# Kernel tuning notes

Measured on AMD Instinct MI355X. Metric: run time of the kernel, lower is better.

## Reference

```python
import jax, jax.numpy as jnp
import numpy as np

# Dimensions
O, D, F_LSOA = 128, 128, 64      # origins, destinations, LSOA feature dim
T, FE, H = 128, 16, 64           # max seq len, edge_feature_dim, gru_hidden
NH, NO, PH = 128, 64, 128        # node_hidden, node_out, pair_hidden
P = O * D                        # number of O-D pairs


def _mlp3(x, W1, b1, W2, b2, W3, b3):
    # Linear->ReLU->Linear->ReLU->Linear (dropout is identity in eval mode)
    h = jax.nn.relu(x @ W1 + b1)
    h = jax.nn.relu(h @ W2 + b2)
    return h @ W3 + b3


def setup_inputs() -> dict:
    key = jax.random.key(0)
    ks = jax.random.split(key, 32)

    def rn(k, shape, s):
        return jax.random.normal(k, shape, dtype=jnp.float32) * s

    inp = {
        "O_feats": rn(ks[0], (O, F_LSOA), 1.0),
        "D_feats": rn(ks[1], (D, F_LSOA), 1.0),
        "seqs": rn(ks[2], (P, T, FE), 1.0),
        "lengths": jax.random.randint(ks[3], (P,), 1, T + 1, dtype=jnp.int32),
        # enc_O
        "WO1": rn(ks[4], (F_LSOA, NH), 0.05), "bO1": jnp.zeros((NH,), jnp.float32),
        "WO2": rn(ks[5], (NH, NH), 0.05),     "bO2": jnp.zeros((NH,), jnp.float32),
        "WO3": rn(ks[6], (NH, NO), 0.05),     "bO3": jnp.zeros((NO,), jnp.float32),
        # enc_D
        "WD1": rn(ks[7], (F_LSOA, NH), 0.05), "bD1": jnp.zeros((NH,), jnp.float32),
        "WD2": rn(ks[8], (NH, NH), 0.05),     "bD2": jnp.zeros((NH,), jnp.float32),
        "WD3": rn(ks[9], (NH, NO), 0.05),     "bD3": jnp.zeros((NO,), jnp.float32),
        # pair_head: 2*node_out -> pair_hidden -> 1
        "Wp1": rn(ks[10], (2 * NO, PH), 0.05), "bp1": jnp.zeros((PH,), jnp.float32),
        "Wp2": rn(ks[11], (PH, 1), 0.05),      "bp2": jnp.zeros((1,), jnp.float32),
        # GRU (gate order r, z, n as in PyTorch)
        "W_ih": rn(ks[12], (FE, 3 * H), 0.1),  "b_ih": jnp.zeros((3 * H,), jnp.float32),
        "W_hh": rn(ks[13], (H, 3 * H), 0.1),   "b_hh": jnp.zeros((3 * H,), jnp.float32),
        # seq_head
        "Ws": rn(ks[14], (H, 1), 0.1),         "bs": jnp.zeros((1,), jnp.float32),
    }
    return inp


def reference(O_feats, D_feats, seqs, lengths,
              WO1, bO1, WO2, bO2, WO3, bO3,
              WD1, bD1, WD2, bD2, WD3, bD3,
              Wp1, bp1, Wp2, bp2,
              W_ih, W_hh, b_ih, b_hh,
              Ws, bs):
    # Node encoders
    eo = _mlp3(O_feats, WO1, bO1, WO2, bO2, WO3, bO3)   # [O, NO]
    ed = _mlp3(D_feats, WD1, bD1, WD2, bD2, WD3, bD3)   # [D, NO]

    # Pairwise score: concat(eo, ed) -> MLP -> softplus
    pair_in = jnp.concatenate([
        jnp.broadcast_to(eo[:, None, :], (O, D, NO)),
        jnp.broadcast_to(ed[None, :, :], (O, D, NO)),
    ], axis=-1)                                          # [O, D, 2*NO]
    hp = jax.nn.relu(pair_in @ Wp1 + bp1)                # [O, D, PH]
    z_pair = (hp @ Wp2 + bp2)[..., 0]                    # [O, D]
    s_pair = jax.nn.softplus(z_pair)

    # Length-masked GRU over all O*D padded sequences (equiv. to pack_padded)
    xT = jnp.swapaxes(seqs, 0, 1)                        # [T, P, FE]
    h0 = jnp.zeros((P, H), jnp.float32)

    def step(h, inp):
        xt, t = inp
        gx = xt @ W_ih + b_ih                            # [P, 3H]
        gh = h @ W_hh + b_hh                             # [P, 3H]
        xr, xz, xn = jnp.split(gx, 3, axis=-1)
        hr, hz, hn = jnp.split(gh, 3, axis=-1)
        r = jax.nn.sigmoid(xr + hr)
        zg = jax.nn.sigmoid(xz + hz)
        n = jnp.tanh(xn + r * hn)
        h_new = (1.0 - zg) * n + zg * h
        h = jnp.where((t < lengths)[:, None], h_new, h)  # freeze past seq end
        return h, None

    h_last, _ = jax.lax.scan(step, h0, (xT, jnp.arange(T)))  # [P, H]

    p_seq = jax.nn.sigmoid(h_last @ Ws + bs)[:, 0].reshape(O, D)
    return jnp.sum(s_pair * p_seq)
```

## Files before the change

### kernel.cpp

```cpp
#include <hip/hip_runtime.h>
#include <hip/hip_bf16.h>

#define O_N 128
#define D_N 128
#define F_LS 64
#define T_MAX 128
#define FE_N 16
#define H_GRU 64
#define NH 128
#define NO 64
#define PH 128
#define NG 1024

typedef _Float16 f16;
typedef f16 f16x8 __attribute__((ext_vector_type(8)));
typedef float f32x4 __attribute__((ext_vector_type(4)));

__device__ __forceinline__ float fast_sigmoid(float x) {
    return __builtin_amdgcn_rcpf(1.f + __expf(-x));
}

__global__ __launch_bounds__(128) void k_enc(
    const float* __restrict__ O_feats, const float* __restrict__ D_feats,
    const float* __restrict__ WO1, const float* __restrict__ bO1,
    const float* __restrict__ WO2, const float* __restrict__ bO2,
    const float* __restrict__ WO3, const float* __restrict__ bO3,
    const float* __restrict__ WD1, const float* __restrict__ bD1,
    const float* __restrict__ WD2, const float* __restrict__ bD2,
    const float* __restrict__ WD3, const float* __restrict__ bD3,
    const float* __restrict__ Wp1,
    float* __restrict__ PA, float* __restrict__ PB, float* __restrict__ d_out)
{
    __shared__ float h1[NH];
    __shared__ float h2[NH];
    __shared__ float ev[NO];
    const int b = blockIdx.x;
    const int enc = b >> 7;
    const int row = b & 127;
    const int t = threadIdx.x;
    if (b == 0 && t == 0) d_out[0] = 0.f;

    const float* x  = (enc ? D_feats : O_feats) + row * F_LS;
    const float* W1 = enc ? WD1 : WO1;  const float* b1 = enc ? bD1 : bO1;
    const float* W2 = enc ? WD2 : WO2;  const float* b2 = enc ? bD2 : bO2;
    const float* W3 = enc ? WD3 : WO3;  const float* b3 = enc ? bD3 : bO3;

    float a = b1[t];
    #pragma unroll 8
    for (int k = 0; k < F_LS; ++k) a += x[k] * W1[k * NH + t];
    h1[t] = fmaxf(a, 0.f);
    __syncthreads();

    a = b2[t];
    #pragma unroll 8
    for (int k = 0; k < NH; ++k) a += h1[k] * W2[k * NH + t];
    h2[t] = fmaxf(a, 0.f);
    __syncthreads();

    if (t < NO) {
        a = b3[t];
        #pragma unroll 8
        for (int k = 0; k < NH; ++k) a += h2[k] * W3[k * NO + t];
        ev[t] = a;
    }
    __syncthreads();

    const float* Wp = Wp1 + (enc ? NO * PH : 0);
    a = 0.f;
    #pragma unroll 8
    for (int k = 0; k < NO; ++k) a += ev[k] * Wp[k * PH + t];
    (enc ? PB : PA)[row * PH + t] = a;
}

__global__ __launch_bounds__(128) void k_pair(
    const float* __restrict__ PA, const float* __restrict__ PB,
    const float* __restrict__ bp1, const float* __restrict__ Wp2,
    const float* __restrict__ bp2, float* __restrict__ s_pair)
{
    const int i = blockIdx.x;
    const int j = threadIdx.x;
    __shared__ float pa[PH];
    __shared__ float b1s[PH];
    __shared__ float w2s[PH];
    pa[j]  = PA[i * PH + j];
    b1s[j] = bp1[j];
    w2s[j] = Wp2[j];
    __syncthreads();
    const float* pb = PB + j * PH;
    float acc = 0.f;
    #pragma unroll 8
    for (int c = 0; c < PH; ++c)
        acc += w2s[c] * fmaxf(pa[c] + pb[c] + b1s[c], 0.f);
    float z = acc + bp2[0];
    float sp = fmaxf(z, 0.f) + log1pf(__expf(-fabsf(z)));
    s_pair[i * 128 + j] = sp;
}

__global__ __launch_bounds__(1024) void k_sort(
    const int* __restrict__ lengths, int* __restrict__ perm)
{
    __shared__ int cnt[130];
    __shared__ int suf[130];
    const int t = threadIdx.x;
    if (t < 130) cnt[t] = 0;
    __syncthreads();
    for (int i = t; i < 16384; i += 1024) atomicAdd(&cnt[lengths[i]], 1);
    __syncthreads();
    if (t < 130) suf[t] = cnt[t];
    __syncthreads();
    for (int d = 1; d < 130; d <<= 1) {
        int v = 0;
        if (t < 130) { v = suf[t]; if (t + d < 130) v += suf[t + d]; }
        __syncthreads();
        if (t < 130) suf[t] = v;
        __syncthreads();
    }
    if (t < 129) cnt[t] = (t + 1 < 130) ? suf[t + 1] : 0;
    __syncthreads();
    for (int i = t; i < 16384; i += 1024) {
        int pos = atomicAdd(&cnt[lengths[i]], 1);
        perm[pos] = i;
    }
}

__global__ __launch_bounds__(256, 4) void k_gru(
    const float* __restrict__ seqs, const int* __restrict__ lengths,
    const int* __restrict__ perm,
    const float* __restrict__ W_ih, const float* __restrict__ b_ih,
    const float* __restrict__ W_hh, const float* __restrict__ b_hh,
    const float* __restrict__ Ws, const float* __restrict__ bs,
    const float* __restrict__ s_pair, float* __restrict__ d_out)
{
    __shared__ __align__(16) f16 hbuf[2 * 1152];
    __shared__ float red[64];
    const int tid = threadIdx.x;
    const int w  = tid >> 6;
    const int l  = tid & 63;
    const int q  = l >> 4;
    const int n  = l & 15;
    const int c  = w * 16 + n;
    const int pb = blockIdx.x * 16;
    const float S_RZ = -1.4426950408889634f;
    const float S_N  =  2.8853900817779268f;

    f16x8 wh[3][2], wi[3];
    #pragma unroll
    for (int g = 0; g < 3; ++g) {
        const int gb = g * 64;
        const float s = (g < 2) ? S_RZ : S_N;
        #pragma unroll
        for (int ks = 0; ks < 2; ++ks)
            #pragma unroll
            for (int j = 0; j < 8; ++j)
                wh[g][ks][j] = (f16)(W_hh[(ks * 32 + q * 8 + j) * 192 + gb + c] * s);
        #pragma unroll
        for (int j = 0; j < 8; ++j) {
            int k = q * 8 + j;
            wi[g][j] = (k < FE_N) ? (f16)(W_ih[k * 192 + gb + c] * s) : (f16)0.f;
        }
    }
    const float brz_r = S_RZ * (b_ih[c] + b_hh[c]);
    const float brz_z = S_RZ * (b_ih[64 + c] + b_hh[64 + c]);
    const float bhn_s = S_N * b_hh[128 + c];
    const float bxn_s = S_N * b_ih[128 + c];
    const f32x4 c_r  = {brz_r, brz_r, brz_r, brz_r};
    const f32x4 c_z  = {brz_z, brz_z, brz_z, brz_z};
    const f32x4 c_hn = {bhn_s, bhn_s, bhn_s, bhn_s};
    const f32x4 c_xn = {bxn_s, bxn_s, bxn_s, bxn_s};
    const float wsc  = Ws[c];
    const float bsv  = bs[0];

    int len[4];
    #pragma unroll
    for (int r = 0; r < 4; ++r) len[r] = lengths[perm[pb + q * 4 + r]];
    int ml = max(max(len[0], len[1]), max(len[2], len[3]));
    ml = max(ml, __shfl_xor(ml, 16));
    ml = max(ml, __shfl_xor(ml, 32));
    const int maxlen = __builtin_amdgcn_readfirstlane(ml);

    {
        f16x8 z8 = {(f16)0, (f16)0, (f16)0, (f16)0, (f16)0, (f16)0, (f16)0, (f16)0};
        if (tid < 144) *(f16x8*)&hbuf[tid * 8] = z8;
    }

    const int pp = perm[pb + n];
    const float4* xp = (const float4*)(seqs + (size_t)pp * (T_MAX * FE_N)) + q * 2;
    float4 xa = {0.f, 0.f, 0.f, 0.f}, xb = xa;
    if (q < 2) { xa = xp[0]; xb = xp[1]; }

    float hold[4] = {0.f, 0.f, 0.f, 0.f};
    const f16x8 zero8 = {(f16)0, (f16)0, (f16)0, (f16)0, (f16)0, (f16)0, (f16)0, (f16)0};
    __syncthreads();

    for (int t = 0; t < maxlen; ++t) {
        f16x8 ax = zero8;
        if (q < 2) {
            ax[0] = (f16)xa.x; ax[1] = (f16)xa.y; ax[2] = (f16)xa.z; ax[3] = (f16)xa.w;
            ax[4] = (f16)xb.x; ax[5] = (f16)xb.y; ax[6] = (f16)xb.z; ax[7] = (f16)xb.w;
            int tn = (t + 1 < maxlen) ? (t + 1) : t;
            xa = xp[tn * 4];
            xb = xp[tn * 4 + 1];
        }
        const f16* hb  = hbuf + (t & 1) * 1152;
        f16*       hbn = hbuf + ((t + 1) & 1) * 1152;

        f16x8 ah0 = *(const f16x8*)&hb[n * 72 + q * 8];
        f16x8 ah1 = *(const f16x8*)&hb[n * 72 + 32 + q * 8];

        f32x4 ar = __builtin_amdgcn_mfma_f32_16x16x32_f16(ah0, wh[0][0], c_r, 0, 0, 0);
        ar = __builtin_amdgcn_mfma_f32_16x16x32_f16(ah1, wh[0][1], ar, 0, 0, 0);
        ar = __builtin_amdgcn_mfma_f32_16x16x32_f16(ax,  wi[0],    ar, 0, 0, 0);
        f32x4 az = __builtin_amdgcn_mfma_f32_16x16x32_f16(ah0, wh[1][0], c_z, 0, 0, 0);
        az = __builtin_amdgcn_mfma_f32_16x16x32_f16(ah1, wh[1][1], az, 0, 0, 0);
        az = __builtin_amdgcn_mfma_f32_16x16x32_f16(ax,  wi[1],    az, 0, 0, 0);
        f32x4 hn = __builtin_amdgcn_mfma_f32_16x16x32_f16(ah0, wh[2][0], c_hn, 0, 0, 0);
        hn = __builtin_amdgcn_mfma_f32_16x16x32_f16(ah1, wh[2][1], hn, 0, 0, 0);
        f32x4 xn = __builtin_amdgcn_mfma_f32_16x16x32_f16(ax, wi[2], c_xn, 0, 0, 0);

        #pragma unroll
        for (int r = 0; r < 4; ++r) {
            float rg    = __builtin_amdgcn_rcpf(1.f + __builtin_amdgcn_exp2f(ar[r]));
            float zg    = __builtin_amdgcn_rcpf(1.f + __builtin_amdgcn_exp2f(az[r]));
            float inner = fmaf(rg, hn[r], xn[r]);
            float nn    = fmaf(-2.f, __builtin_amdgcn_rcpf(1.f + __builtin_amdgcn_exp2f(inner)), 1.f);
            float hv    = hold[r];
            float hnew  = fmaf(zg, hv - nn, nn);
            hnew = (t < len[r]) ? hnew : hv;
            hold[r] = hnew;
            hbn[(q * 4 + r) * 72 + c] = (f16)hnew;
        }
        __syncthreads();
    }

    float part[4];
    #pragma unroll
    for (int r = 0; r < 4; ++r) part[r] = hold[r] * wsc;
    #pragma unroll
    for (int off = 1; off < 16; off <<= 1)
        #pragma unroll
        for (int r = 0; r < 4; ++r)
            part[r] += __shfl_xor(part[r], off);
    if (n == 0) {
        #pragma unroll
        for (int r = 0; r < 4; ++r) red[w * 16 + q * 4 + r] = part[r];
    }
    __syncthreads();
    if (tid < 16) {
        float s = red[tid] + red[16 + tid] + red[32 + tid] + red[48 + tid];
        float pv = fast_sigmoid(s + bsv);
        float contrib = s_pair[perm[pb + tid]] * pv;
        #pragma unroll
        for (int off = 1; off < 16; off <<= 1)
            contrib += __shfl_xor(contrib, off);
        if (tid == 0) atomicAdd(d_out, contrib);
    }
}

extern "C" void kernel_launch(void* const* d_in, const int* in_sizes, int n_in,
                              void* d_out, int out_size, void* d_ws, size_t ws_size,
                              hipStream_t stream)
{
    const float* O_feats = (const float*)d_in[0];
    const float* D_feats = (const float*)d_in[1];
    const float* seqs    = (const float*)d_in[2];
    const int*   lengths = (const int*)d_in[3];
    const float* WO1 = (const float*)d_in[4];  const float* bO1 = (const float*)d_in[5];
    const float* WO2 = (const float*)d_in[6];  const float* bO2 = (const float*)d_in[7];
    const float* WO3 = (const float*)d_in[8];  const float* bO3 = (const float*)d_in[9];
    const float* WD1 = (const float*)d_in[10]; const float* bD1 = (const float*)d_in[11];
    const float* WD2 = (const float*)d_in[12]; const float* bD2 = (const float*)d_in[13];
    const float* WD3 = (const float*)d_in[14]; const float* bD3 = (const float*)d_in[15];
    const float* Wp1 = (const float*)d_in[16]; const float* bp1 = (const float*)d_in[17];
    const float* Wp2 = (const float*)d_in[18]; const float* bp2 = (const float*)d_in[19];
    const float* W_ih = (const float*)d_in[20]; const float* b_ih = (const float*)d_in[21];
    const float* W_hh = (const float*)d_in[22]; const float* b_hh = (const float*)d_in[23];
    const float* Ws   = (const float*)d_in[24]; const float* bs   = (const float*)d_in[25];

    float* out    = (float*)d_out;
    float* PA     = (float*)d_ws;
    float* PB     = PA + 128 * 128;
    float* s_pair = PB + 128 * 128;
    int*   perm   = (int*)(s_pair + 16384);

    k_enc<<<256, 128, 0, stream>>>(O_feats, D_feats,
                                   WO1, bO1, WO2, bO2, WO3, bO3,
                                   WD1, bD1, WD2, bD2, WD3, bD3,
                                   Wp1, PA, PB, out);
    k_pair<<<128, 128, 0, stream>>>(PA, PB, bp1, Wp2, bp2, s_pair);
    k_sort<<<1, 1024, 0, stream>>>(lengths, perm);
    k_gru<<<1024, 256, 0, stream>>>(seqs, lengths, perm, W_ih, b_ih, W_hh, b_hh,
                                    Ws, bs, s_pair, out);
}
```

Baseline: 372.0 us.

## Transpose GRU MFMA so each lane owns one sequence with packed hidden writes

Swaps the MFMA operand order so the accumulator holds four hidden columns of a single sequence per lane instead of four sequences for one column. Each lane now needs only its own length for masking, writes its four f16 hidden values with one 8-byte LDS store instead of four scalar stores, and the final Ws reduction needs fewer shuffles. The time loop is also unrolled by two so the double-buffer indices become compile-time constants. The cost is that biases and Ws become per-register vectors, and the different LDS store pattern could change bank conflicts.

```diff
diff --git a/kernel.cpp b/kernel.cpp
--- a/kernel.cpp
+++ b/kernel.cpp
@@ -13,6 +13,7 @@
 #define NG 1024
 
 typedef _Float16 f16;
+typedef f16 f16x4 __attribute__((ext_vector_type(4)));
 typedef f16 f16x8 __attribute__((ext_vector_type(8)));
 typedef float f32x4 __attribute__((ext_vector_type(4)));
 
@@ -131,7 +132,7 @@
     const float* __restrict__ Ws, const float* __restrict__ bs,
     const float* __restrict__ s_pair, float* __restrict__ d_out)
 {
-    __shared__ __align__(16) f16 hbuf[2 * 1152];
+    __shared__ __align__(16) f16 hbuf[2][16 * 72];
     __shared__ float red[64];
     const int tid = threadIdx.x;
     const int w  = tid >> 6;
@@ -139,6 +140,7 @@
     const int q  = l >> 4;
     const int n  = l & 15;
     const int c  = w * 16 + n;
+    const int colbase = w * 16 + q * 4;
     const int pb = blockIdx.x * 16;
     const float S_RZ = -1.4426950408889634f;
     const float S_N  =  2.8853900817779268f;
@@ -159,32 +161,32 @@
             wi[g][j] = (k < FE_N) ? (f16)(W_ih[k * 192 + gb + c] * s) : (f16)0.f;
         }
     }
-    const float brz_r = S_RZ * (b_ih[c] + b_hh[c]);
-    const float brz_z = S_RZ * (b_ih[64 + c] + b_hh[64 + c]);
-    const float bhn_s = S_N * b_hh[128 + c];
-    const float bxn_s = S_N * b_ih[128 + c];
-    const f32x4 c_r  = {brz_r, brz_r, brz_r, brz_r};
-    const f32x4 c_z  = {brz_z, brz_z, brz_z, brz_z};
-    const f32x4 c_hn = {bhn_s, bhn_s, bhn_s, bhn_s};
-    const f32x4 c_xn = {bxn_s, bxn_s, bxn_s, bxn_s};
-    const float wsc  = Ws[c];
-    const float bsv  = bs[0];
-
-    int len[4];
+    f32x4 c_r, c_z, c_hn, c_xn;
+    float wsc[4];
     #pragma unroll
-    for (int r = 0; r < 4; ++r) len[r] = lengths[perm[pb + q * 4 + r]];
-    int ml = max(max(len[0], len[1]), max(len[2], len[3]));
-    ml = max(ml, __shfl_xor(ml, 16));
-    ml = max(ml, __shfl_xor(ml, 32));
+    for (int r = 0; r < 4; ++r) {
+        int col = colbase + r;
+        c_r[r]  = S_RZ * (b_ih[col] + b_hh[col]);
+        c_z[r]  = S_RZ * (b_ih[64 + col] + b_hh[64 + col]);
+        c_hn[r] = S_N * b_hh[128 + col];
+        c_xn[r] = S_N * b_ih[128 + col];
+        wsc[r]  = Ws[col];
+    }
+    const int myp   = perm[pb + n];
+    const int mylen = lengths[myp];
+    int ml = mylen;
+    ml = max(ml, __shfl_xor(ml, 1));
+    ml = max(ml, __shfl_xor(ml, 2));
+    ml = max(ml, __shfl_xor(ml, 4));
+    ml = max(ml, __shfl_xor(ml, 8));
     const int maxlen = __builtin_amdgcn_readfirstlane(ml);
 
     {
         f16x8 z8 = {(f16)0, (f16)0, (f16)0, (f16)0, (f16)0, (f16)0, (f16)0, (f16)0};
-        if (tid < 144) *(f16x8*)&hbuf[tid * 8] = z8;
-    }
-
-    const int pp = perm[pb + n];
-    const float4* xp = (const float4*)(seqs + (size_t)pp * (T_MAX * FE_N)) + q * 2;
+        if (tid < 144) *(f16x8*)&hbuf[0][tid * 8] = z8;
+    }
+
+    const float4* xp = (const float4*)(seqs + (size_t)myp * (T_MAX * FE_N)) + q * 2;
     float4 xa = {0.f, 0.f, 0.f, 0.f}, xb = xa;
     if (q < 2) { xa = xp[0]; xb = xp[1]; }
 
@@ -192,62 +194,65 @@
     const f16x8 zero8 = {(f16)0, (f16)0, (f16)0, (f16)0, (f16)0, (f16)0, (f16)0, (f16)0};
     __syncthreads();
 
-    for (int t = 0; t < maxlen; ++t) {
-        f16x8 ax = zero8;
-        if (q < 2) {
-            ax[0] = (f16)xa.x; ax[1] = (f16)xa.y; ax[2] = (f16)xa.z; ax[3] = (f16)xa.w;
-            ax[4] = (f16)xb.x; ax[5] = (f16)xb.y; ax[6] = (f16)xb.z; ax[7] = (f16)xb.w;
-            int tn = (t + 1 < maxlen) ? (t + 1) : t;
-            xa = xp[tn * 4];
-            xb = xp[tn * 4 + 1];
+    #pragma unroll 1
+    for (int t = 0; t < maxlen; t += 2) {
+        #pragma unroll
+        for (int sub = 0; sub < 2; ++sub) {
+            const int tt = t + sub;
+            if (sub == 1 && tt >= maxlen) break;
+            const f16* hb  = hbuf[sub];
+            f16*       hbw = hbuf[sub ^ 1];
+
+            f16x8 ax = zero8;
+            if (q < 2) {
+                ax[0] = (f16)xa.x; ax[1] = (f16)xa.y; ax[2] = (f16)xa.z; ax[3] = (f16)xa.w;
+                ax[4] = (f16)xb.x; ax[5] = (f16)xb.y; ax[6] = (f16)xb.z; ax[7] = (f16)xb.w;
+                int tn = (tt + 1 < maxlen) ? (tt + 1) : tt;
+                xa = xp[tn * 4];
+                xb = xp[tn * 4 + 1];
+            }
+            f16x8 bh0 = *(const f16x8*)&hb[n * 72 + 8 * q];
+            f16x8 bh1 = *(const f16x8*)&hb[n * 72 + 32 + 8 * q];
+
+            f32x4 ar = __builtin_amdgcn_mfma_f32_16x16x32_f16(wh[0][0], bh0, c_r, 0, 0, 0);
+            ar = __builtin_amdgcn_mfma_f32_16x16x32_f16(wh[0][1], bh1, ar, 0, 0, 0);
+            ar = __builtin_amdgcn_mfma_f32_16x16x32_f16(wi[0],    ax,  ar, 0, 0, 0);
+            f32x4 az = __builtin_amdgcn_mfma_f32_16x16x32_f16(wh[1][0], bh0, c_z, 0, 0, 0);
+            az = __builtin_amdgcn_mfma_f32_16x16x32_f16(wh[1][1], bh1, az, 0, 0, 0);
+            az = __builtin_amdgcn_mfma_f32_16x16x32_f16(wi[1],    ax,  az, 0, 0, 0);
+            f32x4 hn = __builtin_amdgcn_mfma_f32_16x16x32_f16(wh[2][0], bh0, c_hn, 0, 0, 0);
+            hn = __builtin_amdgcn_mfma_f32_16x16x32_f16(wh[2][1], bh1, hn, 0, 0, 0);
+            f32x4 xn = __builtin_amdgcn_mfma_f32_16x16x32_f16(wi[2], ax, c_xn, 0, 0, 0);
+
+            const bool live = (tt < mylen);
+            #pragma unroll
+            for (int r = 0; r < 4; ++r) {
+                float rg    = __builtin_amdgcn_rcpf(1.f + __builtin_amdgcn_exp2f(ar[r]));
+                float zg    = __builtin_amdgcn_rcpf(1.f + __builtin_amdgcn_exp2f(az[r]));
+                float inner = fmaf(rg, hn[r], xn[r]);
+                float nn    = fmaf(-2.f, __builtin_amdgcn_rcpf(1.f + __builtin_amdgcn_exp2f(inner)), 1.f);
+                float hnew  = fmaf(zg, hold[r] - nn, nn);
+                hold[r] = live ? hnew : hold[r];
+            }
+            f16x4 hv4;
+            hv4[0] = (f16)hold[0];
+            hv4[1] = (f16)hold[1];
+            hv4[2] = (f16)hold[2];
+            hv4[3] = (f16)hold[3];
+            *(f16x4*)&hbw[n * 72 + colbase] = hv4;
+            __syncthreads();
         }
-        const f16* hb  = hbuf + (t & 1) * 1152;
-        f16*       hbn = hbuf + ((t + 1) & 1) * 1152;
-
-        f16x8 ah0 = *(const f16x8*)&hb[n * 72 + q * 8];
-        f16x8 ah1 = *(const f16x8*)&hb[n * 72 + 32 + q * 8];
-
-        f32x4 ar = __builtin_amdgcn_mfma_f32_16x16x32_f16(ah0, wh[0][0], c_r, 0, 0, 0);
-        ar = __builtin_amdgcn_mfma_f32_16x16x32_f16(ah1, wh[0][1], ar, 0, 0, 0);
-        ar = __builtin_amdgcn_mfma_f32_16x16x32_f16(ax,  wi[0],    ar, 0, 0, 0);
-        f32x4 az = __builtin_amdgcn_mfma_f32_16x16x32_f16(ah0, wh[1][0], c_z, 0, 0, 0);
-        az = __builtin_amdgcn_mfma_f32_16x16x32_f16(ah1, wh[1][1], az, 0, 0, 0);
-        az = __builtin_amdgcn_mfma_f32_16x16x32_f16(ax,  wi[1],    az, 0, 0, 0);
-        f32x4 hn = __builtin_amdgcn_mfma_f32_16x16x32_f16(ah0, wh[2][0], c_hn, 0, 0, 0);
-        hn = __builtin_amdgcn_mfma_f32_16x16x32_f16(ah1, wh[2][1], hn, 0, 0, 0);
-        f32x4 xn = __builtin_amdgcn_mfma_f32_16x16x32_f16(ax, wi[2], c_xn, 0, 0, 0);
-
-        #pragma unroll
-        for (int r = 0; r < 4; ++r) {
-            float rg    = __builtin_amdgcn_rcpf(1.f + __builtin_amdgcn_exp2f(ar[r]));
-            float zg    = __builtin_amdgcn_rcpf(1.f + __builtin_amdgcn_exp2f(az[r]));
-            float inner = fmaf(rg, hn[r], xn[r]);
-            float nn    = fmaf(-2.f, __builtin_amdgcn_rcpf(1.f + __builtin_amdgcn_exp2f(inner)), 1.f);
-            float hv    = hold[r];
-            float hnew  = fmaf(zg, hv - nn, nn);
-            hnew = (t < len[r]) ? hnew : hv;
-            hold[r] = hnew;
-            hbn[(q * 4 + r) * 72 + c] = (f16)hnew;
-        }
-        __syncthreads();
-    }
-
-    float part[4];
-    #pragma unroll
-    for (int r = 0; r < 4; ++r) part[r] = hold[r] * wsc;
-    #pragma unroll
-    for (int off = 1; off < 16; off <<= 1)
-        #pragma unroll
-        for (int r = 0; r < 4; ++r)
-            part[r] += __shfl_xor(part[r], off);
-    if (n == 0) {
-        #pragma unroll
-        for (int r = 0; r < 4; ++r) red[w * 16 + q * 4 + r] = part[r];
-    }
+    }
+
+    float part = hold[0] * wsc[0] + hold[1] * wsc[1] +
+                 hold[2] * wsc[2] + hold[3] * wsc[3];
+    part += __shfl_xor(part, 16);
+    part += __shfl_xor(part, 32);
+    if (l < 16) red[w * 16 + n] = part;
     __syncthreads();
     if (tid < 16) {
         float s = red[tid] + red[16 + tid] + red[32 + tid] + red[48 + tid];
-        float pv = fast_sigmoid(s + bsv);
+        float pv = fast_sigmoid(s + bs[0]);
         float contrib = s_pair[perm[pb + tid]] * pv;
         #pragma unroll
         for (int off = 1; off < 16; off <<= 1)
```

Measured after the change: 365.6 us. About the same (-1.7%).
